# Kernel tuning notes

Hardware: AMD Instinct MI355X
Metric: run time of the kernel (lower is better)

The kernel has to match this reference:

```python
import jax, jax.numpy as jnp
import numpy as np

# metaLinearLayer: per-sample weight W_b = left^T @ diag(meta_b) @ right.
# torch builds diag(meta)@eye@left then transposes and matmuls right, i.e.
# meta_weight[b] = (diag(meta_b) @ left).T @ right, shape (input_dim, out_dim).
# We apply it via associativity: (x @ left^T) * meta, then @ right -- same math,
# skipping the dense per-sample weight.

B, S, D_IN, D_OUT, P = 8, 4096, 2048, 2048, 256

def setup_inputs() -> dict:
    key = jax.random.key(0)
    ks = jax.random.split(key, 6)
    scale_l = (6.0 / D_IN) ** 0.5   # kaiming_uniform-ish magnitude
    scale_r = (6.0 / P) ** 0.5
    return {
        "input": jax.random.normal(ks[0], (B, S, D_IN), dtype=jnp.float32),
        "meta_input": jax.random.normal(ks[1], (B, P), dtype=jnp.float32),
        "left": jax.random.uniform(ks[2], (P, D_IN), dtype=jnp.float32, minval=-scale_l, maxval=scale_l),
        "right": jax.random.uniform(ks[3], (P, D_OUT), dtype=jnp.float32, minval=-scale_r, maxval=scale_r),
        "bias_w": jax.random.uniform(ks[4], (P, D_OUT), dtype=jnp.float32, minval=-scale_r, maxval=scale_r),
        "bias_b": jax.random.uniform(ks[5], (D_OUT,), dtype=jnp.float32, minval=-scale_r, maxval=scale_r),
    }

def reference(input, meta_input, left, right, bias_w, bias_b):
    # project input to rank-P space: [B,S,P]
    h = jnp.einsum('bsj,pj->bsp', input, left)
    # per-sample diagonal scaling by meta_input
    h = h * meta_input[:, None, :]
    # project to out_dim: [B,S,out_dim]
    out = jnp.einsum('bsp,pk->bsk', h, right)
    # meta bias = project2bias(meta_input), broadcast over seq
    meta_bias = meta_input @ bias_w + bias_b  # [B, out_dim]
    return out + meta_bias[:, None, :]
```

## Files before the change

kernel.cpp:

```cpp
#include <hip/hip_runtime.h>
#include <hip/hip_bf16.h>
#include <stdint.h>

#define B_    8
#define S_    4096
#define DIN   2048
#define DOUT  2048
#define P_    256
#define M_    (B_ * S_)

typedef __attribute__((ext_vector_type(4))) float f32x4;
typedef __attribute__((ext_vector_type(8))) short bf16x8;

static __device__ __forceinline__ short f2bs(float x) {
    __hip_bfloat16 h = __float2bfloat16(x);
    return *reinterpret_cast<short*>(&h);
}

static __device__ __forceinline__ void gld_lds16(const void* g, void* l) {
    __builtin_amdgcn_global_load_lds(
        (const __attribute__((address_space(1))) unsigned int*)(uintptr_t)g,
        (__attribute__((address_space(3))) unsigned int*)(uintptr_t)l,
        16, 0, 0);
}

#define SWZ(row, byteoff) ((byteoff) ^ (((row) & 7) << 4))

__global__ __launch_bounds__(256)
void prep_left(const float* __restrict__ L, char* __restrict__ Lsw) {
    int g = blockIdx.x * 256 + threadIdx.x;
    int row = g >> 8;
    int c8  = g & 255;
    int k = c8 * 8, kt = k >> 6, kk = k & 63;
    const float* src = L + (size_t)row * DIN + k;
    float4 v0 = *reinterpret_cast<const float4*>(src);
    float4 v1 = *reinterpret_cast<const float4*>(src + 4);
    bf16x8 o;
    o[0]=f2bs(v0.x); o[1]=f2bs(v0.y); o[2]=f2bs(v0.z); o[3]=f2bs(v0.w);
    o[4]=f2bs(v1.x); o[5]=f2bs(v1.y); o[6]=f2bs(v1.z); o[7]=f2bs(v1.w);
    int off = kt * 32768 + SWZ(row, row * 128 + kk * 2);
    *reinterpret_cast<bf16x8*>(Lsw + off) = o;
}

__global__ __launch_bounds__(256)
void prep_right(const float* __restrict__ R, char* __restrict__ Rsw) {
    __shared__ float T[64][65];
    const int n0 = blockIdx.x * 64;
    const int p0 = blockIdx.y * 64;
    const int tid = threadIdx.x;
    #pragma unroll
    for (int e = 0; e < 16; ++e) {
        int idx = tid + e * 256;
        int r = idx >> 6, c = idx & 63;
        T[r][c] = R[(size_t)(p0 + r) * DOUT + n0 + c];
    }
    __syncthreads();
    #pragma unroll
    for (int e = 0; e < 2; ++e) {
        int cc = tid + e * 256;
        int nl = cc >> 3, p8 = (cc & 7) * 8;
        bf16x8 o;
        #pragma unroll
        for (int u = 0; u < 8; ++u) o[u] = f2bs(T[p8 + u][nl]);
        int n = n0 + nl;
        int nb = n >> 8, row = n & 255;
        int kt = p0 >> 6, kk = p8;
        int off = (nb * 4 + kt) * 32768 + SWZ(row, row * 128 + kk * 2);
        *reinterpret_cast<bf16x8*>(Rsw + off) = o;
    }
}

__global__ __launch_bounds__(256)
void meta_bias_kernel(const float* __restrict__ meta,
                      const float* __restrict__ bias_w,
                      const float* __restrict__ bias_b,
                      float* __restrict__ mb) {
    int g = blockIdx.x * 256 + threadIdx.x;
    int b  = g >> 9;
    int k4 = (g & 511) * 4;
    const float* mrow = meta + b * P_;
    float4 acc = *reinterpret_cast<const float4*>(&bias_b[k4]);
    #pragma unroll 4
    for (int p = 0; p < P_; ++p) {
        float mval = mrow[p];
        float4 wv = *reinterpret_cast<const float4*>(&bias_w[(size_t)p * DOUT + k4]);
        acc.x = fmaf(mval, wv.x, acc.x);
        acc.y = fmaf(mval, wv.y, acc.y);
        acc.z = fmaf(mval, wv.z, acc.z);
        acc.w = fmaf(mval, wv.w, acc.w);
    }
    *reinterpret_cast<float4*>(&mb[(size_t)b * DOUT + k4]) = acc;
}

template<bool S1>
__global__ __launch_bounds__(256, 3)
void gemm_mfma(const void* __restrict__ Ap,
               const char* __restrict__ Bsw,
               const float* __restrict__ vvec,
               void* __restrict__ Cp) {
    constexpr int KTOT = S1 ? DIN : P_;
    constexpr int NK   = KTOT / 64;
    __shared__ short As[64 * 64];
    __shared__ short Bs[256 * 64];

    const int tid  = threadIdx.x;
    const int lane = tid & 63;
    const int w    = tid >> 6;
    const int lm   = lane & 15;
    const int rg   = lane >> 4;
    const int mblk = blockIdx.x;
    const int r0   = mblk * 64;
    const int c0   = S1 ? 0 : blockIdx.y * 256;
    const int bidx = mblk >> 6;

    f32x4 acc[4][4] = {};
    const float* Xf  = (const float*)Ap;
    const char* Himg = (const char*)Ap;
    char* AsB = (char*)As;
    char* BsB = (char*)Bs;

    for (int kt = 0; kt < NK; ++kt) {
        const char* bimg = Bsw + (size_t)(S1 ? kt : ((int)blockIdx.y * NK + kt)) * 32768;
        #pragma unroll
        for (int c = 0; c < 8; ++c)
            gld_lds16(bimg + (w * 8 + c) * 1024 + lane * 16, BsB + (w * 8 + c) * 1024);
        if (S1) {
            #pragma unroll
            for (int e = 0; e < 2; ++e) {
                int row = (tid >> 3) + e * 32;
                int k8  = (tid & 7) * 8;
                const float* src = Xf + (size_t)(r0 + row) * DIN + kt * 64 + k8;
                float4 v0 = *reinterpret_cast<const float4*>(src);
                float4 v1 = *reinterpret_cast<const float4*>(src + 4);
                bf16x8 o;
                o[0]=f2bs(v0.x); o[1]=f2bs(v0.y); o[2]=f2bs(v0.z); o[3]=f2bs(v0.w);
                o[4]=f2bs(v1.x); o[5]=f2bs(v1.y); o[6]=f2bs(v1.z); o[7]=f2bs(v1.w);
                *reinterpret_cast<bf16x8*>(AsB + SWZ(row, row * 128 + k8 * 2)) = o;
            }
        } else {
            const char* aimg = Himg + ((size_t)mblk * NK + kt) * 8192;
            #pragma unroll
            for (int c = 0; c < 2; ++c)
                gld_lds16(aimg + (w * 2 + c) * 1024 + lane * 16, AsB + (w * 2 + c) * 1024);
        }
        __syncthreads();

        #pragma unroll
        for (int kk = 0; kk < 2; ++kk) {
            bf16x8 af[4], bfr[4];
            #pragma unroll
            for (int i = 0; i < 4; ++i) {
                int m = i * 16 + lm;
                af[i] = *reinterpret_cast<const bf16x8*>(
                    AsB + SWZ(m, m * 128 + (kk * 32 + rg * 8) * 2));
            }
            #pragma unroll
            for (int j = 0; j < 4; ++j) {
                int n = w * 64 + j * 16 + lm;
                bfr[j] = *reinterpret_cast<const bf16x8*>(
                    BsB + SWZ(n, n * 128 + (kk * 32 + rg * 8) * 2));
            }
            #pragma unroll
            for (int i = 0; i < 4; ++i)
                #pragma unroll
                for (int j = 0; j < 4; ++j)
                    acc[i][j] = __builtin_amdgcn_mfma_f32_16x16x32_bf16(
                        af[i], bfr[j], acc[i][j], 0, 0, 0);
        }
        __syncthreads();
    }

    if (S1) {
        const float* mrow = vvec + bidx * P_;
        char* Hout = (char*)Cp + (size_t)mblk * 32768;
        float mv[4];
        #pragma unroll
        for (int j = 0; j < 4; ++j) mv[j] = mrow[w * 64 + j * 16 + lm];
        #pragma unroll
        for (int i = 0; i < 4; ++i) {
            int rb = i * 16 + rg * 4;
            #pragma unroll
            for (int j = 0; j < 4; ++j) {
                int p = w * 64 + j * 16 + lm;
                int ktile = p >> 6, kk = p & 63;
                #pragma unroll
                for (int q = 0; q < 4; ++q) {
                    int r = rb + q;
                    int off = ktile * 8192 + SWZ(r, r * 128 + kk * 2);
                    *reinterpret_cast<short*>(Hout + off) = f2bs(acc[i][j][q] * mv[j]);
                }
            }
        }
    } else {
        const float* mbr = vvec + bidx * DOUT;
        float* Oc = (float*)Cp;
        float bv[4];
        #pragma unroll
        for (int j = 0; j < 4; ++j) bv[j] = mbr[c0 + w * 64 + j * 16 + lm];
        #pragma unroll
        for (int i = 0; i < 4; ++i) {
            #pragma unroll
            for (int j = 0; j < 4; ++j) {
                int col = c0 + w * 64 + j * 16 + lm;
                #pragma unroll
                for (int q = 0; q < 4; ++q) {
                    int row = r0 + i * 16 + rg * 4 + q;
                    Oc[(size_t)row * DOUT + col] = acc[i][j][q] + bv[j];
                }
            }
        }
    }
}

extern "C" void kernel_launch(void* const* d_in, const int* in_sizes, int n_in,
                              void* d_out, int out_size, void* d_ws, size_t ws_size,
                              hipStream_t stream) {
    const float* input  = (const float*)d_in[0];
    const float* meta   = (const float*)d_in[1];
    const float* left   = (const float*)d_in[2];
    const float* right  = (const float*)d_in[3];
    const float* bias_w = (const float*)d_in[4];
    const float* bias_b = (const float*)d_in[5];
    float* out = (float*)d_out;

    char* ws  = (char*)d_ws;
    char* Hsw = ws;
    float* mb = (float*)(ws + 16777216);
    char* Lsw = ws + 16777216 + 65536;
    char* Rsw = Lsw + 1048576;

    prep_left <<<256, 256, 0, stream>>>(left, Lsw);
    prep_right<<<dim3(DOUT / 64, P_ / 64), 256, 0, stream>>>(right, Rsw);
    meta_bias_kernel<<<16, 256, 0, stream>>>(meta, bias_w, bias_b, mb);

    gemm_mfma<true><<<dim3(M_ / 64, 1), 256, 0, stream>>>(input, Lsw, meta, Hsw);

    gemm_mfma<false><<<dim3(M_ / 64, DOUT / 256), 256, 0, stream>>>(Hsw, Rsw, mb, out);
}
```

Baseline: 569.0 us.

## Read B operands directly from global and double-buffer A tiles in GEMM1

The shared templated GEMM is split into two kernels. The B operand (bf16 left and transposed right) is no longer staged through LDS; each lane loads its fragments straight from global/L2. GEMM1 also double-buffers the A tile in LDS and prefetches the next fp32 input chunk into registers while the MFMAs run, so each k-step needs only one barrier. This cuts LDS traffic and barrier stalls, but relies on L2 to serve the redundant B reads from every block. It also raises register use, which is why GEMM1's occupancy target drops to 2.

```diff
diff --git a/kernel.cpp b/kernel.cpp
--- a/kernel.cpp
+++ b/kernel.cpp
@@ -11,6 +11,7 @@
 
 typedef __attribute__((ext_vector_type(4))) float f32x4;
 typedef __attribute__((ext_vector_type(8))) short bf16x8;
+typedef __attribute__((ext_vector_type(4))) short bf16x4;
 
 static __device__ __forceinline__ short f2bs(float x) {
     __hip_bfloat16 h = __float2bfloat16(x);
@@ -27,23 +28,18 @@
 #define SWZ(row, byteoff) ((byteoff) ^ (((row) & 7) << 4))
 
 __global__ __launch_bounds__(256)
-void prep_left(const float* __restrict__ L, char* __restrict__ Lsw) {
-    int g = blockIdx.x * 256 + threadIdx.x;
-    int row = g >> 8;
-    int c8  = g & 255;
-    int k = c8 * 8, kt = k >> 6, kk = k & 63;
-    const float* src = L + (size_t)row * DIN + k;
-    float4 v0 = *reinterpret_cast<const float4*>(src);
-    float4 v1 = *reinterpret_cast<const float4*>(src + 4);
+void cvt_left(const float* __restrict__ src, short* __restrict__ dst) {
+    int i = blockIdx.x * 256 + threadIdx.x;
+    const float4* s = reinterpret_cast<const float4*>(src) + (size_t)i * 2;
+    float4 a = s[0], b = s[1];
     bf16x8 o;
-    o[0]=f2bs(v0.x); o[1]=f2bs(v0.y); o[2]=f2bs(v0.z); o[3]=f2bs(v0.w);
-    o[4]=f2bs(v1.x); o[5]=f2bs(v1.y); o[6]=f2bs(v1.z); o[7]=f2bs(v1.w);
-    int off = kt * 32768 + SWZ(row, row * 128 + kk * 2);
-    *reinterpret_cast<bf16x8*>(Lsw + off) = o;
+    o[0]=f2bs(a.x); o[1]=f2bs(a.y); o[2]=f2bs(a.z); o[3]=f2bs(a.w);
+    o[4]=f2bs(b.x); o[5]=f2bs(b.y); o[6]=f2bs(b.z); o[7]=f2bs(b.w);
+    *(reinterpret_cast<bf16x8*>(dst) + i) = o;
 }
 
 __global__ __launch_bounds__(256)
-void prep_right(const float* __restrict__ R, char* __restrict__ Rsw) {
+void transposeR(const float* __restrict__ R, short* __restrict__ Rt) {
     __shared__ float T[64][65];
     const int n0 = blockIdx.x * 64;
     const int p0 = blockIdx.y * 64;
@@ -56,52 +52,35 @@
     }
     __syncthreads();
     #pragma unroll
-    for (int e = 0; e < 2; ++e) {
-        int cc = tid + e * 256;
-        int nl = cc >> 3, p8 = (cc & 7) * 8;
-        bf16x8 o;
-        #pragma unroll
-        for (int u = 0; u < 8; ++u) o[u] = f2bs(T[p8 + u][nl]);
-        int n = n0 + nl;
-        int nb = n >> 8, row = n & 255;
-        int kt = p0 >> 6, kk = p8;
-        int off = (nb * 4 + kt) * 32768 + SWZ(row, row * 128 + kk * 2);
-        *reinterpret_cast<bf16x8*>(Rsw + off) = o;
+    for (int e = 0; e < 4; ++e) {
+        int g = tid + e * 256;
+        int n = g >> 4, p4 = (g & 15) << 2;
+        bf16x4 v;
+        v[0] = f2bs(T[p4 + 0][n]); v[1] = f2bs(T[p4 + 1][n]);
+        v[2] = f2bs(T[p4 + 2][n]); v[3] = f2bs(T[p4 + 3][n]);
+        *reinterpret_cast<bf16x4*>(&Rt[(size_t)(n0 + n) * P_ + p0 + p4]) = v;
     }
 }
 
 __global__ __launch_bounds__(256)
-void meta_bias_kernel(const float* __restrict__ meta,
-                      const float* __restrict__ bias_w,
-                      const float* __restrict__ bias_b,
-                      float* __restrict__ mb) {
-    int g = blockIdx.x * 256 + threadIdx.x;
-    int b  = g >> 9;
-    int k4 = (g & 511) * 4;
+void meta_bias(const float* __restrict__ meta,
+               const float* __restrict__ bias_w,
+               const float* __restrict__ bias_b,
+               float* __restrict__ mb) {
+    int b = blockIdx.x >> 3;
+    int k = (blockIdx.x & 7) * 256 + threadIdx.x;
     const float* mrow = meta + b * P_;
-    float4 acc = *reinterpret_cast<const float4*>(&bias_b[k4]);
-    #pragma unroll 4
-    for (int p = 0; p < P_; ++p) {
-        float mval = mrow[p];
-        float4 wv = *reinterpret_cast<const float4*>(&bias_w[(size_t)p * DOUT + k4]);
-        acc.x = fmaf(mval, wv.x, acc.x);
-        acc.y = fmaf(mval, wv.y, acc.y);
-        acc.z = fmaf(mval, wv.z, acc.z);
-        acc.w = fmaf(mval, wv.w, acc.w);
-    }
-    *reinterpret_cast<float4*>(&mb[(size_t)b * DOUT + k4]) = acc;
-}
-
-template<bool S1>
-__global__ __launch_bounds__(256, 3)
-void gemm_mfma(const void* __restrict__ Ap,
-               const char* __restrict__ Bsw,
-               const float* __restrict__ vvec,
-               void* __restrict__ Cp) {
-    constexpr int KTOT = S1 ? DIN : P_;
-    constexpr int NK   = KTOT / 64;
-    __shared__ short As[64 * 64];
-    __shared__ short Bs[256 * 64];
+    float acc = bias_b[k];
+    #pragma unroll 8
+    for (int p = 0; p < P_; ++p)
+        acc = fmaf(mrow[p], bias_w[(size_t)p * DOUT + k], acc);
+    mb[(size_t)b * DOUT + k] = acc;
+}
+
+__global__ __launch_bounds__(256, 2)
+void gemm1(const float* __restrict__ X, const short* __restrict__ Lb,
+           const float* __restrict__ meta, char* __restrict__ Hsw) {
+    __shared__ short As[2][64 * 64];
 
     const int tid  = threadIdx.x;
     const int lane = tid & 63;
@@ -110,103 +89,147 @@
     const int rg   = lane >> 4;
     const int mblk = blockIdx.x;
     const int r0   = mblk * 64;
-    const int c0   = S1 ? 0 : blockIdx.y * 256;
     const int bidx = mblk >> 6;
 
+    const int row_s = tid >> 2;
+    const int kq    = (tid & 3) * 16;
+    const float* xbase = X + (size_t)(r0 + row_s) * DIN + kq;
+    const int wsw0 = SWZ(row_s, row_s * 128 + kq * 2);
+    const int wsw1 = SWZ(row_s, row_s * 128 + kq * 2 + 16);
+
     f32x4 acc[4][4] = {};
-    const float* Xf  = (const float*)Ap;
-    const char* Himg = (const char*)Ap;
-    char* AsB = (char*)As;
-    char* BsB = (char*)Bs;
-
-    for (int kt = 0; kt < NK; ++kt) {
-        const char* bimg = Bsw + (size_t)(S1 ? kt : ((int)blockIdx.y * NK + kt)) * 32768;
-        #pragma unroll
-        for (int c = 0; c < 8; ++c)
-            gld_lds16(bimg + (w * 8 + c) * 1024 + lane * 16, BsB + (w * 8 + c) * 1024);
-        if (S1) {
-            #pragma unroll
-            for (int e = 0; e < 2; ++e) {
-                int row = (tid >> 3) + e * 32;
-                int k8  = (tid & 7) * 8;
-                const float* src = Xf + (size_t)(r0 + row) * DIN + kt * 64 + k8;
-                float4 v0 = *reinterpret_cast<const float4*>(src);
-                float4 v1 = *reinterpret_cast<const float4*>(src + 4);
-                bf16x8 o;
-                o[0]=f2bs(v0.x); o[1]=f2bs(v0.y); o[2]=f2bs(v0.z); o[3]=f2bs(v0.w);
-                o[4]=f2bs(v1.x); o[5]=f2bs(v1.y); o[6]=f2bs(v1.z); o[7]=f2bs(v1.w);
-                *reinterpret_cast<bf16x8*>(AsB + SWZ(row, row * 128 + k8 * 2)) = o;
-            }
-        } else {
-            const char* aimg = Himg + ((size_t)mblk * NK + kt) * 8192;
-            #pragma unroll
-            for (int c = 0; c < 2; ++c)
-                gld_lds16(aimg + (w * 2 + c) * 1024 + lane * 16, AsB + (w * 2 + c) * 1024);
-        }
+    float4 xr0, xr1, xr2, xr3;
+    {
+        const float4* s = reinterpret_cast<const float4*>(xbase);
+        xr0 = s[0]; xr1 = s[1]; xr2 = s[2]; xr3 = s[3];
+    }
+
+    for (int kt = 0; kt < 32; ++kt) {
+        char* asb = (char*)As[kt & 1];
+        bf16x8 o0, o1;
+        o0[0]=f2bs(xr0.x); o0[1]=f2bs(xr0.y); o0[2]=f2bs(xr0.z); o0[3]=f2bs(xr0.w);
+        o0[4]=f2bs(xr1.x); o0[5]=f2bs(xr1.y); o0[6]=f2bs(xr1.z); o0[7]=f2bs(xr1.w);
+        o1[0]=f2bs(xr2.x); o1[1]=f2bs(xr2.y); o1[2]=f2bs(xr2.z); o1[3]=f2bs(xr2.w);
+        o1[4]=f2bs(xr3.x); o1[5]=f2bs(xr3.y); o1[6]=f2bs(xr3.z); o1[7]=f2bs(xr3.w);
+        *reinterpret_cast<bf16x8*>(asb + wsw0) = o0;
+        *reinterpret_cast<bf16x8*>(asb + wsw1) = o1;
         __syncthreads();
 
+        if (kt < 31) {
+            const float4* s = reinterpret_cast<const float4*>(xbase + (kt + 1) * 64);
+            xr0 = s[0]; xr1 = s[1]; xr2 = s[2]; xr3 = s[3];
+        }
+
+        bf16x8 bfr[4][2];
+        #pragma unroll
+        for (int j = 0; j < 4; ++j)
+            #pragma unroll
+            for (int kk = 0; kk < 2; ++kk)
+                bfr[j][kk] = *reinterpret_cast<const bf16x8*>(
+                    Lb + (size_t)(w * 64 + j * 16 + lm) * DIN + kt * 64 + kk * 32 + rg * 8);
+
         #pragma unroll
         for (int kk = 0; kk < 2; ++kk) {
-            bf16x8 af[4], bfr[4];
+            bf16x8 af[4];
             #pragma unroll
             for (int i = 0; i < 4; ++i) {
                 int m = i * 16 + lm;
                 af[i] = *reinterpret_cast<const bf16x8*>(
-                    AsB + SWZ(m, m * 128 + (kk * 32 + rg * 8) * 2));
-            }
-            #pragma unroll
-            for (int j = 0; j < 4; ++j) {
-                int n = w * 64 + j * 16 + lm;
-                bfr[j] = *reinterpret_cast<const bf16x8*>(
-                    BsB + SWZ(n, n * 128 + (kk * 32 + rg * 8) * 2));
+                    asb + SWZ(m, m * 128 + (kk * 32 + rg * 8) * 2));
             }
             #pragma unroll
             for (int i = 0; i < 4; ++i)
                 #pragma unroll
                 for (int j = 0; j < 4; ++j)
                     acc[i][j] = __builtin_amdgcn_mfma_f32_16x16x32_bf16(
-                        af[i], bfr[j], acc[i][j], 0, 0, 0);
-        }
+                        af[i], bfr[j][kk], acc[i][j], 0, 0, 0);
+        }
+    }
+
+    const float* mrow = meta + bidx * P_;
+    char* hb = Hsw + (size_t)mblk * 32768 + w * 8192;
+    float mv[4];
+    #pragma unroll
+    for (int j = 0; j < 4; ++j) mv[j] = mrow[w * 64 + j * 16 + lm];
+    #pragma unroll
+    for (int i = 0; i < 4; ++i) {
+        #pragma unroll
+        for (int j = 0; j < 4; ++j) {
+            int kk2 = j * 16 + lm;
+            #pragma unroll
+            for (int q = 0; q < 4; ++q) {
+                int r = i * 16 + rg * 4 + q;
+                *reinterpret_cast<short*>(hb + SWZ(r, r * 128 + kk2 * 2)) =
+                    f2bs(acc[i][j][q] * mv[j]);
+            }
+        }
+    }
+}
+
+__global__ __launch_bounds__(256, 3)
+void gemm2(const char* __restrict__ Hsw, const short* __restrict__ Rt,
+           const float* __restrict__ mb, float* __restrict__ O) {
+    __shared__ short As[64 * 64];
+
+    const int tid  = threadIdx.x;
+    const int lane = tid & 63;
+    const int w    = tid >> 6;
+    const int lm   = lane & 15;
+    const int rg   = lane >> 4;
+    const int mblk = blockIdx.x;
+    const int r0   = mblk * 64;
+    const int c0   = blockIdx.y * 256;
+    const int bidx = mblk >> 6;
+    char* asb = (char*)As;
+
+    f32x4 acc[4][4] = {};
+
+    for (int kt = 0; kt < 4; ++kt) {
+        const char* aimg = Hsw + ((size_t)mblk * 4 + kt) * 8192;
+        gld_lds16(aimg + (w * 2 + 0) * 1024 + lane * 16, asb + (w * 2 + 0) * 1024);
+        gld_lds16(aimg + (w * 2 + 1) * 1024 + lane * 16, asb + (w * 2 + 1) * 1024);
         __syncthreads();
-    }
-
-    if (S1) {
-        const float* mrow = vvec + bidx * P_;
-        char* Hout = (char*)Cp + (size_t)mblk * 32768;
-        float mv[4];
-        #pragma unroll
-        for (int j = 0; j < 4; ++j) mv[j] = mrow[w * 64 + j * 16 + lm];
-        #pragma unroll
-        for (int i = 0; i < 4; ++i) {
-            int rb = i * 16 + rg * 4;
-            #pragma unroll
-            for (int j = 0; j < 4; ++j) {
-                int p = w * 64 + j * 16 + lm;
-                int ktile = p >> 6, kk = p & 63;
+
+        bf16x8 bfr[4][2];
+        #pragma unroll
+        for (int j = 0; j < 4; ++j)
+            #pragma unroll
+            for (int kk = 0; kk < 2; ++kk)
+                bfr[j][kk] = *reinterpret_cast<const bf16x8*>(
+                    Rt + (size_t)(c0 + w * 64 + j * 16 + lm) * P_ + kt * 64 + kk * 32 + rg * 8);
+
+        #pragma unroll
+        for (int kk = 0; kk < 2; ++kk) {
+            bf16x8 af[4];
+            #pragma unroll
+            for (int i = 0; i < 4; ++i) {
+                int m = i * 16 + lm;
+                af[i] = *reinterpret_cast<const bf16x8*>(
+                    asb + SWZ(m, m * 128 + (kk * 32 + rg * 8) * 2));
+            }
+            #pragma unroll
+            for (int i = 0; i < 4; ++i)
                 #pragma unroll
-                for (int q = 0; q < 4; ++q) {
-                    int r = rb + q;
-                    int off = ktile * 8192 + SWZ(r, r * 128 + kk * 2);
-                    *reinterpret_cast<short*>(Hout + off) = f2bs(acc[i][j][q] * mv[j]);
-                }
-            }
-        }
-    } else {
-        const float* mbr = vvec + bidx * DOUT;
-        float* Oc = (float*)Cp;
-        float bv[4];
-        #pragma unroll
-        for (int j = 0; j < 4; ++j) bv[j] = mbr[c0 + w * 64 + j * 16 + lm];
-        #pragma unroll
-        for (int i = 0; i < 4; ++i) {
-            #pragma unroll
-            for (int j = 0; j < 4; ++j) {
-                int col = c0 + w * 64 + j * 16 + lm;
-                #pragma unroll
-                for (int q = 0; q < 4; ++q) {
-                    int row = r0 + i * 16 + rg * 4 + q;
-                    Oc[(size_t)row * DOUT + col] = acc[i][j][q] + bv[j];
-                }
+                for (int j = 0; j < 4; ++j)
+                    acc[i][j] = __builtin_amdgcn_mfma_f32_16x16x32_bf16(
+                        af[i], bfr[j][kk], acc[i][j], 0, 0, 0);
+        }
+        __syncthreads();
+    }
+
+    const float* mbr = mb + (size_t)bidx * DOUT;
+    float bv[4];
+    #pragma unroll
+    for (int j = 0; j < 4; ++j) bv[j] = mbr[c0 + w * 64 + j * 16 + lm];
+    #pragma unroll
+    for (int i = 0; i < 4; ++i) {
+        #pragma unroll
+        for (int j = 0; j < 4; ++j) {
+            int col = c0 + w * 64 + j * 16 + lm;
+            #pragma unroll
+            for (int q = 0; q < 4; ++q) {
+                int row = r0 + i * 16 + rg * 4 + q;
+                O[(size_t)row * DOUT + col] = acc[i][j][q] + bv[j];
             }
         }
     }
@@ -226,14 +249,13 @@
     char* ws  = (char*)d_ws;
     char* Hsw = ws;
     float* mb = (float*)(ws + 16777216);
-    char* Lsw = ws + 16777216 + 65536;
-    char* Rsw = Lsw + 1048576;
-
-    prep_left <<<256, 256, 0, stream>>>(left, Lsw);
-    prep_right<<<dim3(DOUT / 64, P_ / 64), 256, 0, stream>>>(right, Rsw);
-    meta_bias_kernel<<<16, 256, 0, stream>>>(meta, bias_w, bias_b, mb);
-
-    gemm_mfma<true><<<dim3(M_ / 64, 1), 256, 0, stream>>>(input, Lsw, meta, Hsw);
-
-    gemm_mfma<false><<<dim3(M_ / 64, DOUT / 256), 256, 0, stream>>>(Hsw, Rsw, mb, out);
-}
+    short* Lb = (short*)(ws + 16777216 + 65536);
+    short* Rt = (short*)(ws + 16777216 + 65536 + 1048576);
+
+    cvt_left  <<<256, 256, 0, stream>>>(left, Lb);
+    transposeR<<<dim3(DOUT / 64, P_ / 64), 256, 0, stream>>>(right, Rt);
+    meta_bias <<<64, 256, 0, stream>>>(meta, bias_w, bias_b, mb);
+
+    gemm1<<<dim3(M_ / 64), 256, 0, stream>>>(input, Lb, meta, Hsw);
+    gemm2<<<dim3(M_ / 64, DOUT / 256), 256, 0, stream>>>(Hsw, Rt, mb, out);
+}
```

Result: slower. 597.0 us (+4.9%).
